# Kernel tuning notes

Measured on AMD Instinct MI355X. Metric: run time of the kernel, lower is better.

The kernel has to match this reference:

```python
import jax, jax.numpy as jnp
import numpy as np

B, T, V, E, U = 32, 512, 8000, 256, 512


def _lstm(x, mask, Wk, Wr, b):
    """Keras-semantics masked LSTM. x:[B,T,D], mask:[B,T] bool -> [B,T,U].
    At masked steps the state is not updated and the output carries the
    previous hidden state (Keras K.rnn default, zero_output_for_mask=False)."""
    xW = jnp.einsum('btd,dk->btk', x, Wk) + b  # precompute input projections [B,T,4U]
    units = Wr.shape[0]

    def step(carry, inp):
        h, c = carry
        xw, m = inp  # xw:[B,4U], m:[B]
        z = xw + h @ Wr
        i, f, g, o = jnp.split(z, 4, axis=-1)  # Keras gate order i,f,c,o
        c_new = jax.nn.sigmoid(f) * c + jax.nn.sigmoid(i) * jnp.tanh(g)
        h_new = jax.nn.sigmoid(o) * jnp.tanh(c_new)
        m2 = m[:, None]
        h_new = jnp.where(m2, h_new, h)
        c_new = jnp.where(m2, c_new, c)
        return (h_new, c_new), h_new

    h0 = jnp.zeros((x.shape[0], units), x.dtype)
    _, ys = jax.lax.scan(step, (h0, h0), (jnp.swapaxes(xW, 0, 1), mask.T))
    return jnp.swapaxes(ys, 0, 1)


def _bidir(x, mask, kf, rf, bf, kb, rb, bb):
    fwd = _lstm(x, mask, kf, rf, bf)
    bwd = _lstm(x[:, ::-1], mask[:, ::-1], kb, rb, bb)[:, ::-1]
    return jnp.concatenate([fwd, bwd], axis=-1)


def setup_inputs() -> dict:
    key = jax.random.key(0)
    ks = jax.random.split(key, 12)
    s = 0.05  # glorot-ish scale for stability through tanh/sigmoid
    return {
        'tokens': jax.random.randint(ks[0], (B, T), 0, V, dtype=jnp.int32),
        'emb': jax.random.normal(ks[1], (V, E), jnp.float32) * s,
        'k1f': jax.random.normal(ks[2], (E, 4 * U), jnp.float32) * s,
        'r1f': jax.random.normal(ks[3], (U, 4 * U), jnp.float32) * s,
        'b1f': jnp.zeros((4 * U,), jnp.float32),
        'k1b': jax.random.normal(ks[4], (E, 4 * U), jnp.float32) * s,
        'r1b': jax.random.normal(ks[5], (U, 4 * U), jnp.float32) * s,
        'b1b': jnp.zeros((4 * U,), jnp.float32),
        'k2f': jax.random.normal(ks[6], (2 * U, 4 * U), jnp.float32) * s,
        'r2f': jax.random.normal(ks[7], (U, 4 * U), jnp.float32) * s,
        'b2f': jnp.zeros((4 * U,), jnp.float32),
        'k2b': jax.random.normal(ks[8], (2 * U, 4 * U), jnp.float32) * s,
        'r2b': jax.random.normal(ks[9], (U, 4 * U), jnp.float32) * s,
        'b2b': jnp.zeros((4 * U,), jnp.float32),
        'wd': jax.random.normal(ks[10], (2 * U, V), jnp.float32) * s,
        'bd': jnp.zeros((V,), jnp.float32),
    }


def reference(tokens, emb, k1f, r1f, b1f, k1b, r1b, b1b,
              k2f, r2f, b2f, k2b, r2b, b2b, wd, bd):
    mask = tokens != 0  # Embedding(mask_zero=True)
    x = emb[tokens]  # [B,T,E]
    h1 = _bidir(x, mask, k1f, r1f, b1f, k1b, r1b, b1b)  # [B,T,2U]; Dropout is identity at inference
    h2 = _bidir(h1, mask, k2f, r2f, b2f, k2b, r2b, b2b)  # [B,T,2U]
    logits = jnp.einsum('btd,dv->btv', h2, wd) + bd  # [B,T,V]
    return logits
```

## Files before the change

kernel.cpp:

```cpp
#include <hip/hip_runtime.h>
#include <hip/hip_bf16.h>
#include <stdint.h>

#define B_   32
#define T_   512
#define V_   8000
#define E_   256
#define U_   512
#define BT_  (B_*T_)
#define G4_  (4*U_)
#define GWG  32
#define UPW  (U_/GWG)

typedef unsigned short ushort_t;
typedef __attribute__((ext_vector_type(8))) short   short8;
typedef __attribute__((ext_vector_type(4))) float   floatx4;

__device__ __forceinline__ float bf2f(ushort_t u) {
    union { unsigned int i; float f; } v; v.i = ((unsigned int)u) << 16; return v.f;
}
__device__ __forceinline__ ushort_t f2bf(float f) {
    union { float f; unsigned int i; } v; v.f = f;
    unsigned int r = v.i + 0x7fffu + ((v.i >> 16) & 1u);
    return (ushort_t)(r >> 16);
}
__device__ __forceinline__ float sigmoidf_(float x) { return 1.0f / (1.0f + __expf(-x)); }
__device__ __forceinline__ float tanhf_(float x) {
    float ax = fabsf(x);
    float e  = __expf(-2.0f * ax);
    float r  = (1.0f - e) / (1.0f + e);
    return copysignf(r, x);
}

__device__ __forceinline__ void stg_h_sc1(ushort_t* p, unsigned int v) {
    asm volatile("global_store_short %0, %1, off sc0 sc1"
                 :: "v"(p), "v"(v) : "memory");
}
template<int OFFB>
__device__ __forceinline__ short8 ldg_h_sc1(const ushort_t* p) {
    short8 r;
    asm volatile("global_load_dwordx4 %0, %1, off offset:%2 sc0 sc1"
                 : "=&v"(r) : "v"(p), "i"(OFFB));
    return r;
}

__global__ void embed_kernel(const int* __restrict__ tokens,
                             const float* __restrict__ emb,
                             ushort_t* __restrict__ x)
{
    int row = blockIdx.x * 4 + (threadIdx.x >> 6);
    int col = (threadIdx.x & 63) * 4;
    int tok = tokens[row];
    const float4 v = *(const float4*)(emb + (size_t)tok * E_ + col);
    ushort_t* dst = x + (size_t)row * E_ + col;
    dst[0] = f2bf(v.x); dst[1] = f2bf(v.y); dst[2] = f2bf(v.z); dst[3] = f2bf(v.w);
}

__global__ void transpose_f32_bf16(const float* __restrict__ in,
                                   ushort_t* __restrict__ out, int R, int C)
{
    __shared__ ushort_t tile[32][33];
    int c0 = blockIdx.x * 32, r0 = blockIdx.y * 32;
    int r = threadIdx.x >> 3;
    int c4 = (threadIdx.x & 7) * 4;
    const float* src = in + (size_t)(r0 + r) * C + c0 + c4;
    #pragma unroll
    for (int i = 0; i < 4; ++i) tile[r][c4 + i] = f2bf(src[i]);
    __syncthreads();
    ushort_t* dst = out + (size_t)(c0 + r) * R + r0 + c4;
    #pragma unroll
    for (int i = 0; i < 4; ++i) dst[i] = tile[c4 + i][r];
}

template <bool OUT_F32>
__global__ __launch_bounds__(256)
void gemm_bt(const ushort_t* __restrict__ A,
             const ushort_t* __restrict__ BT,
             const float* __restrict__ bias,
             void* __restrict__ Cv,
             int M, int Nd, int K)
{
    const int tid = threadIdx.x, lane = tid & 63, wave = tid >> 6;
    const int wm = wave >> 1, wn = wave & 1;
    const int m0 = blockIdx.x * 128;
    const int n0 = blockIdx.y * 128;
    __shared__ __align__(16) ushort_t As[128 * 32];
    __shared__ __align__(16) ushort_t Bs[128 * 32];
    floatx4 acc[4][4];
    #pragma unroll
    for (int i = 0; i < 4; ++i)
        #pragma unroll
        for (int j = 0; j < 4; ++j) acc[i][j] = (floatx4){0.f, 0.f, 0.f, 0.f};

    const int lr = lane >> 2;
    const int lk = (lane & 3) * 8;
    const int rowL = wave * 32 + lr;
    const int ra0 = m0 + rowL;
    int rb0 = n0 + rowL;      if (rb0 > Nd - 1) rb0 = Nd - 1;
    int rb1 = n0 + rowL + 16; if (rb1 > Nd - 1) rb1 = Nd - 1;

    for (int k0 = 0; k0 < K; k0 += 32) {
        uint4 a0 = *(const uint4*)(A  + (size_t)ra0        * K + k0 + lk);
        uint4 a1 = *(const uint4*)(A  + (size_t)(ra0 + 16) * K + k0 + lk);
        uint4 b0 = *(const uint4*)(BT + (size_t)rb0        * K + k0 + lk);
        uint4 b1 = *(const uint4*)(BT + (size_t)rb1        * K + k0 + lk);
        __syncthreads();
        *(uint4*)(As + (rowL     ) * 32 + lk) = a0;
        *(uint4*)(As + (rowL + 16) * 32 + lk) = a1;
        *(uint4*)(Bs + (rowL     ) * 32 + lk) = b0;
        *(uint4*)(Bs + (rowL + 16) * 32 + lk) = b1;
        __syncthreads();
        short8 af[4], bw[4];
        #pragma unroll
        for (int i = 0; i < 4; ++i)
            af[i] = *(const short8*)(As + (wm * 64 + i * 16 + (lane & 15)) * 32 + (lane >> 4) * 8);
        #pragma unroll
        for (int j = 0; j < 4; ++j)
            bw[j] = *(const short8*)(Bs + (wn * 64 + j * 16 + (lane & 15)) * 32 + (lane >> 4) * 8);
        #pragma unroll
        for (int i = 0; i < 4; ++i)
            #pragma unroll
            for (int j = 0; j < 4; ++j)
                acc[i][j] = __builtin_amdgcn_mfma_f32_16x16x32_bf16(af[i], bw[j], acc[i][j], 0, 0, 0);
    }
    #pragma unroll
    for (int j = 0; j < 4; ++j) {
        int n = n0 + wn * 64 + j * 16 + (lane & 15);
        bool nok = (n < Nd);
        float bv = nok ? bias[nok ? n : 0] : 0.f;
        #pragma unroll
        for (int i = 0; i < 4; ++i) {
            #pragma unroll
            for (int r = 0; r < 4; ++r) {
                int m = m0 + wm * 64 + i * 16 + (lane >> 4) * 4 + r;
                if (nok) {
                    float v = acc[i][j][r] + bv;
                    if (OUT_F32) ((float*)Cv)[(size_t)m * Nd + n] = v;
                    else         ((ushort_t*)Cv)[(size_t)m * Nd + n] = f2bf(v);
                }
            }
        }
    }
}

__global__ __launch_bounds__(512)
void lstm_rec(const ushort_t* __restrict__ xw,
              const ushort_t* __restrict__ WrTf,
              const ushort_t* __restrict__ WrTb,
              const int* __restrict__ tokens,
              ushort_t* __restrict__ h,
              int* __restrict__ cnt)
{
    const int tid  = threadIdx.x;
    const int lane = tid & 63;
    const int wave = tid >> 6;
    const int dir  = blockIdx.y;
    const int g    = blockIdx.x;
    const int mt   = wave >> 2;
    const int q    = wave & 3;
    const int l16  = lane & 15;
    const int l4   = lane >> 4;
    const ushort_t* WrT = dir ? WrTb : WrTf;

    short8 bfrag[16];
    {
        const ushort_t* src = WrT + (size_t)(q * U_ + g * UPW + l16) * U_ + l4 * 8;
        #pragma unroll
        for (int kb = 0; kb < 16; ++kb) bfrag[kb] = *(const short8*)(src + kb * 32);
    }

    __shared__ float zs[4][32][17];

    const int b_me = tid >> 4;
    const int u_me = tid & 15;
    const int u_g  = g * UPW + u_me;
    float c_st = 0.0f, h_st = 0.0f;
    const int cbase = dir * T_;

    for (int s = 0; s < T_; ++s) {
        const int t = dir ? (T_ - 1 - s) : s;
        const ushort_t* xwp = xw + ((size_t)dir * BT_ + (size_t)b_me * T_ + t) * G4_ + u_g;
        ushort_t xwi = xwp[0 * U_], xwf = xwp[1 * U_], xwg = xwp[2 * U_], xwo = xwp[3 * U_];
        int tok = tokens[b_me * T_ + t];

        floatx4 acc = (floatx4){0.f, 0.f, 0.f, 0.f};
        if (s > 0) {
            if (tid == 0) {
                while (__hip_atomic_load(&cnt[cbase + s - 1], __ATOMIC_RELAXED,
                                         __HIP_MEMORY_SCOPE_AGENT) < GWG) { }
            }
            __syncthreads();
            const int tp = dir ? (t + 1) : (t - 1);
            const ushort_t* hp = h + ((size_t)(mt * 16 + l16) * T_ + tp) * (2 * U_)
                                   + dir * U_ + l4 * 8;
            short8 af[16];
            af[0]  = ldg_h_sc1< 0 * 64>(hp);
            af[1]  = ldg_h_sc1< 1 * 64>(hp);
            af[2]  = ldg_h_sc1< 2 * 64>(hp);
            af[3]  = ldg_h_sc1< 3 * 64>(hp);
            af[4]  = ldg_h_sc1< 4 * 64>(hp);
            af[5]  = ldg_h_sc1< 5 * 64>(hp);
            af[6]  = ldg_h_sc1< 6 * 64>(hp);
            af[7]  = ldg_h_sc1< 7 * 64>(hp);
            af[8]  = ldg_h_sc1< 8 * 64>(hp);
            af[9]  = ldg_h_sc1< 9 * 64>(hp);
            af[10] = ldg_h_sc1<10 * 64>(hp);
            af[11] = ldg_h_sc1<11 * 64>(hp);
            af[12] = ldg_h_sc1<12 * 64>(hp);
            af[13] = ldg_h_sc1<13 * 64>(hp);
            af[14] = ldg_h_sc1<14 * 64>(hp);
            af[15] = ldg_h_sc1<15 * 64>(hp);
            asm volatile("s_waitcnt vmcnt(0)" ::: "memory");
            __builtin_amdgcn_sched_barrier(0);
            #pragma unroll
            for (int kb = 0; kb < 16; ++kb)
                acc = __builtin_amdgcn_mfma_f32_16x16x32_bf16(af[kb], bfrag[kb], acc, 0, 0, 0);
        }
        #pragma unroll
        for (int r = 0; r < 4; ++r)
            zs[q][mt * 16 + l4 * 4 + r][l16] = acc[r];
        __syncthreads();

        float zi = bf2f(xwi) + zs[0][b_me][u_me];
        float zf = bf2f(xwf) + zs[1][b_me][u_me];
        float zg = bf2f(xwg) + zs[2][b_me][u_me];
        float zo = bf2f(xwo) + zs[3][b_me][u_me];
        float c_new = sigmoidf_(zf) * c_st + sigmoidf_(zi) * tanhf_(zg);
        float h_new = sigmoidf_(zo) * tanhf_(c_new);
        bool msk = (tok != 0);
        float h_sel = msk ? h_new : h_st;
        float c_sel = msk ? c_new : c_st;
        h_st = h_sel; c_st = c_sel;
        stg_h_sc1(h + ((size_t)b_me * T_ + t) * (2 * U_) + dir * U_ + u_g,
                  (unsigned int)f2bf(h_sel));
        asm volatile("s_waitcnt vmcnt(0)" ::: "memory");
        __syncthreads();
        if (tid == 0)
            __hip_atomic_fetch_add(&cnt[cbase + s], 1, __ATOMIC_RELAXED,
                                   __HIP_MEMORY_SCOPE_AGENT);
    }
}

extern "C" void kernel_launch(void* const* d_in, const int* in_sizes, int n_in,
                              void* d_out, int out_size, void* d_ws, size_t ws_size,
                              hipStream_t stream)
{
    const int*   tokens = (const int*)d_in[0];
    const float* emb  = (const float*)d_in[1];
    const float* k1f  = (const float*)d_in[2];
    const float* r1f  = (const float*)d_in[3];
    const float* b1f  = (const float*)d_in[4];
    const float* k1b  = (const float*)d_in[5];
    const float* r1b  = (const float*)d_in[6];
    const float* b1b  = (const float*)d_in[7];
    const float* k2f  = (const float*)d_in[8];
    const float* r2f  = (const float*)d_in[9];
    const float* b2f  = (const float*)d_in[10];
    const float* k2b  = (const float*)d_in[11];
    const float* r2b  = (const float*)d_in[12];
    const float* b2b  = (const float*)d_in[13];
    const float* wd   = (const float*)d_in[14];
    const float* bd   = (const float*)d_in[15];
    float* out = (float*)d_out;

    const size_t MB = 1024 * 1024;
    ushort_t* xw   = (ushort_t*)d_out;
    ushort_t* x    = (ushort_t*)((char*)d_out + 128 * MB);
    ushort_t* h1   = (ushort_t*)((char*)d_out + 136 * MB);
    char* wb       = (char*)d_out + 168 * MB;
    ushort_t* k1fT = (ushort_t*)(wb);
    ushort_t* k1bT = (ushort_t*)(wb + 1  * MB);
    ushort_t* k2fT = (ushort_t*)(wb + 2  * MB);
    ushort_t* k2bT = (ushort_t*)(wb + 6  * MB);
    ushort_t* r1fT = (ushort_t*)(wb + 10 * MB);
    ushort_t* r1bT = (ushort_t*)(wb + 12 * MB);
    ushort_t* r2fT = (ushort_t*)(wb + 14 * MB);
    ushort_t* r2bT = (ushort_t*)(wb + 16 * MB);
    int*      cnt  = (int*)d_ws;
    ushort_t* h2   = (ushort_t*)((char*)d_ws + 65536);
    ushort_t* wdT  = (ushort_t*)((char*)d_ws + 65536 + (size_t)BT_ * 2 * U_ * 2);

    hipMemsetAsync(cnt, 0, 2 * 2 * T_ * sizeof(int), stream);
    embed_kernel<<<BT_ / 4, 256, 0, stream>>>(tokens, emb, x);

    transpose_f32_bf16<<<dim3(2048/32, 256/32 ), 256, 0, stream>>>(k1f, k1fT, 256,  2048);
    transpose_f32_bf16<<<dim3(2048/32, 256/32 ), 256, 0, stream>>>(k1b, k1bT, 256,  2048);
    transpose_f32_bf16<<<dim3(2048/32, 1024/32), 256, 0, stream>>>(k2f, k2fT, 1024, 2048);
    transpose_f32_bf16<<<dim3(2048/32, 1024/32), 256, 0, stream>>>(k2b, k2bT, 1024, 2048);
    transpose_f32_bf16<<<dim3(2048/32, 512/32 ), 256, 0, stream>>>(r1f, r1fT, 512,  2048);
    transpose_f32_bf16<<<dim3(2048/32, 512/32 ), 256, 0, stream>>>(r1b, r1bT, 512,  2048);
    transpose_f32_bf16<<<dim3(2048/32, 512/32 ), 256, 0, stream>>>(r2f, r2fT, 512,  2048);
    transpose_f32_bf16<<<dim3(2048/32, 512/32 ), 256, 0, stream>>>(r2b, r2bT, 512,  2048);
    transpose_f32_bf16<<<dim3(8000/32, 1024/32), 256, 0, stream>>>(wd,  wdT,  1024, 8000);

    gemm_bt<false><<<dim3(128, 16), 256, 0, stream>>>(x, k1fT, b1f, xw,                      BT_, G4_, E_);
    gemm_bt<false><<<dim3(128, 16), 256, 0, stream>>>(x, k1bT, b1b, xw + (size_t)BT_ * G4_,  BT_, G4_, E_);
    lstm_rec<<<dim3(GWG, 2), 512, 0, stream>>>(xw, r1fT, r1bT, tokens, h1, cnt);
    gemm_bt<false><<<dim3(128, 16), 256, 0, stream>>>(h1, k2fT, b2f, xw,                     BT_, G4_, 2*U_);
    gemm_bt<false><<<dim3(128, 16), 256, 0, stream>>>(h1, k2bT, b2b, xw + (size_t)BT_ * G4_, BT_, G4_, 2*U_);
    lstm_rec<<<dim3(GWG, 2), 512, 0, stream>>>(xw, r2fT, r2bT, tokens, h2, cnt + 2 * T_);
    gemm_bt<true><<<dim3(128, (V_ + 127) / 128), 256, 0, stream>>>(h2, wdT, bd, out, BT_, V_, 2*U_);
}
```

Baseline: 7.249 ms.

## Store gate projections in step-major interleaved layout and trim recurrence barriers

The input-projection GEMM now writes its bf16 output as [t][group][b][u16][gate], so each recurrent thread reads its four gate values for a step with one 8-byte load instead of four scattered 2-byte loads. The recurrent step's per-step feed, which is latency bound, becomes contiguous. The serial MFMA chain is split into four independent accumulators to shorten dependency latency. __syncthreads is replaced by raw s_barrier with explicit waitcnt and sched barriers to cut per-step sync overhead. The GEMM epilogue's scattered stores may be less coalesced.

```diff
diff --git a/kernel.cpp b/kernel.cpp
--- a/kernel.cpp
+++ b/kernel.cpp
@@ -72,7 +72,7 @@
     for (int i = 0; i < 4; ++i) dst[i] = tile[c4 + i][r];
 }
 
-template <bool OUT_F32>
+template <int MODE>
 __global__ __launch_bounds__(256)
 void gemm_bt(const ushort_t* __restrict__ A,
              const ushort_t* __restrict__ BT,
@@ -135,8 +135,20 @@
                 int m = m0 + wm * 64 + i * 16 + (lane >> 4) * 4 + r;
                 if (nok) {
                     float v = acc[i][j][r] + bv;
-                    if (OUT_F32) ((float*)Cv)[(size_t)m * Nd + n] = v;
-                    else         ((ushort_t*)Cv)[(size_t)m * Nd + n] = f2bf(v);
+                    if (MODE == 1) {
+                        ((float*)Cv)[(size_t)m * Nd + n] = v;
+                    } else if (MODE == 0) {
+                        ((ushort_t*)Cv)[(size_t)m * Nd + n] = f2bf(v);
+                    } else {
+                        int t    = m & (T_ - 1);
+                        int b    = m >> 9;
+                        int gate = n >> 9;
+                        int u    = n & 511;
+                        int g    = u >> 4;
+                        int u16  = u & 15;
+                        size_t dst = (size_t)t * 65536 + g * 2048 + b * 64 + u16 * 4 + gate;
+                        ((ushort_t*)Cv)[dst] = f2bf(v);
+                    }
                 }
             }
         }
@@ -176,20 +188,22 @@
     const int u_g  = g * UPW + u_me;
     float c_st = 0.0f, h_st = 0.0f;
     const int cbase = dir * T_;
+    const ushort_t* xbase = xw + (size_t)dir * BT_ * G4_
+                          + (size_t)g * 2048 + (size_t)b_me * 64 + u_me * 4;
 
     for (int s = 0; s < T_; ++s) {
         const int t = dir ? (T_ - 1 - s) : s;
-        const ushort_t* xwp = xw + ((size_t)dir * BT_ + (size_t)b_me * T_ + t) * G4_ + u_g;
-        ushort_t xwi = xwp[0 * U_], xwf = xwp[1 * U_], xwg = xwp[2 * U_], xwo = xwp[3 * U_];
+        ushort4 xv = *(const ushort4*)(xbase + (size_t)t * 65536);
         int tok = tokens[b_me * T_ + t];
 
-        floatx4 acc = (floatx4){0.f, 0.f, 0.f, 0.f};
+        floatx4 acc;
         if (s > 0) {
             if (tid == 0) {
                 while (__hip_atomic_load(&cnt[cbase + s - 1], __ATOMIC_RELAXED,
                                          __HIP_MEMORY_SCOPE_AGENT) < GWG) { }
             }
-            __syncthreads();
+            __builtin_amdgcn_s_barrier();
+            __builtin_amdgcn_sched_barrier(0);
             const int tp = dir ? (t + 1) : (t - 1);
             const ushort_t* hp = h + ((size_t)(mt * 16 + l16) * T_ + tp) * (2 * U_)
                                    + dir * U_ + l4 * 8;
@@ -212,19 +226,29 @@
             af[15] = ldg_h_sc1<15 * 64>(hp);
             asm volatile("s_waitcnt vmcnt(0)" ::: "memory");
             __builtin_amdgcn_sched_barrier(0);
+            floatx4 a0 = (floatx4){0.f,0.f,0.f,0.f}, a1 = a0, a2 = a0, a3 = a0;
             #pragma unroll
-            for (int kb = 0; kb < 16; ++kb)
-                acc = __builtin_amdgcn_mfma_f32_16x16x32_bf16(af[kb], bfrag[kb], acc, 0, 0, 0);
+            for (int kb = 0; kb < 16; kb += 4) {
+                a0 = __builtin_amdgcn_mfma_f32_16x16x32_bf16(af[kb    ], bfrag[kb    ], a0, 0, 0, 0);
+                a1 = __builtin_amdgcn_mfma_f32_16x16x32_bf16(af[kb + 1], bfrag[kb + 1], a1, 0, 0, 0);
+                a2 = __builtin_amdgcn_mfma_f32_16x16x32_bf16(af[kb + 2], bfrag[kb + 2], a2, 0, 0, 0);
+                a3 = __builtin_amdgcn_mfma_f32_16x16x32_bf16(af[kb + 3], bfrag[kb + 3], a3, 0, 0, 0);
+            }
+            acc = (a0 + a1) + (a2 + a3);
+        } else {
+            acc = (floatx4){0.f, 0.f, 0.f, 0.f};
         }
         #pragma unroll
         for (int r = 0; r < 4; ++r)
             zs[q][mt * 16 + l4 * 4 + r][l16] = acc[r];
-        __syncthreads();
-
-        float zi = bf2f(xwi) + zs[0][b_me][u_me];
-        float zf = bf2f(xwf) + zs[1][b_me][u_me];
-        float zg = bf2f(xwg) + zs[2][b_me][u_me];
-        float zo = bf2f(xwo) + zs[3][b_me][u_me];
+        asm volatile("s_waitcnt lgkmcnt(0)" ::: "memory");
+        __builtin_amdgcn_s_barrier();
+        __builtin_amdgcn_sched_barrier(0);
+
+        float zi = bf2f(xv.x) + zs[0][b_me][u_me];
+        float zf = bf2f(xv.y) + zs[1][b_me][u_me];
+        float zg = bf2f(xv.z) + zs[2][b_me][u_me];
+        float zo = bf2f(xv.w) + zs[3][b_me][u_me];
         float c_new = sigmoidf_(zf) * c_st + sigmoidf_(zi) * tanhf_(zg);
         float h_new = sigmoidf_(zo) * tanhf_(c_new);
         bool msk = (tok != 0);
@@ -234,7 +258,8 @@
         stg_h_sc1(h + ((size_t)b_me * T_ + t) * (2 * U_) + dir * U_ + u_g,
                   (unsigned int)f2bf(h_sel));
         asm volatile("s_waitcnt vmcnt(0)" ::: "memory");
-        __syncthreads();
+        __builtin_amdgcn_s_barrier();
+        __builtin_amdgcn_sched_barrier(0);
         if (tid == 0)
             __hip_atomic_fetch_add(&cnt[cbase + s], 1, __ATOMIC_RELAXED,
                                    __HIP_MEMORY_SCOPE_AGENT);
@@ -293,11 +318,11 @@
     transpose_f32_bf16<<<dim3(2048/32, 512/32 ), 256, 0, stream>>>(r2b, r2bT, 512,  2048);
     transpose_f32_bf16<<<dim3(8000/32, 1024/32), 256, 0, stream>>>(wd,  wdT,  1024, 8000);
 
-    gemm_bt<false><<<dim3(128, 16), 256, 0, stream>>>(x, k1fT, b1f, xw,                      BT_, G4_, E_);
-    gemm_bt<false><<<dim3(128, 16), 256, 0, stream>>>(x, k1bT, b1b, xw + (size_t)BT_ * G4_,  BT_, G4_, E_);
+    gemm_bt<2><<<dim3(128, 16), 256, 0, stream>>>(x, k1fT, b1f, xw,                      BT_, G4_, E_);
+    gemm_bt<2><<<dim3(128, 16), 256, 0, stream>>>(x, k1bT, b1b, xw + (size_t)BT_ * G4_,  BT_, G4_, E_);
     lstm_rec<<<dim3(GWG, 2), 512, 0, stream>>>(xw, r1fT, r1bT, tokens, h1, cnt);
-    gemm_bt<false><<<dim3(128, 16), 256, 0, stream>>>(h1, k2fT, b2f, xw,                     BT_, G4_, 2*U_);
-    gemm_bt<false><<<dim3(128, 16), 256, 0, stream>>>(h1, k2bT, b2b, xw + (size_t)BT_ * G4_, BT_, G4_, 2*U_);
+    gemm_bt<2><<<dim3(128, 16), 256, 0, stream>>>(h1, k2fT, b2f, xw,                     BT_, G4_, 2*U_);
+    gemm_bt<2><<<dim3(128, 16), 256, 0, stream>>>(h1, k2bT, b2b, xw + (size_t)BT_ * G4_, BT_, G4_, 2*U_);
     lstm_rec<<<dim3(GWG, 2), 512, 0, stream>>>(xw, r2fT, r2bT, tokens, h2, cnt + 2 * T_);
-    gemm_bt<true><<<dim3(128, (V_ + 127) / 128), 256, 0, stream>>>(h2, wdT, bd, out, BT_, V_, 2*U_);
-}
+    gemm_bt<1><<<dim3(128, (V_ + 127) / 128), 256, 0, stream>>>(h2, wdT, bd, out, BT_, V_, 2*U_);
+}
```

Result: slower. 7.425 ms (+2.4%).
